# Kernel tuning notes

Measured on AMD Instinct MI355X. Metric: run time of the kernel, lower is better.

Reference implementation:

```python
import jax, jax.numpy as jnp
import numpy as np

NEG_INF = -1e9


def setup_inputs() -> dict:
    key = jax.random.key(0)
    ks = jax.random.split(key, 6)
    B, S, E, D = 32, 2048, 1024, 1024
    dec_hidden = jax.random.normal(ks[0], (B, D), dtype=jnp.float32)
    enc_outputs = jax.random.normal(ks[1], (B, S, E), dtype=jnp.float32)
    mask = jax.random.randint(ks[2], (B, S), 0, 2, dtype=jnp.int32)
    # scale weights ~ Glorot-ish so tanh isn't saturated
    W_enc = jax.random.normal(ks[3], (D, E), dtype=jnp.float32) / np.sqrt(E)
    W_dec = jax.random.normal(ks[4], (D, D), dtype=jnp.float32) / np.sqrt(D)
    v = jax.random.normal(ks[5], (D,), dtype=jnp.float32) / np.sqrt(D)
    return {"dec_hidden": dec_hidden, "enc_outputs": enc_outputs, "mask": mask,
            "W_enc": W_enc, "W_dec": W_dec, "v": v}


def reference(dec_hidden, enc_outputs, mask, W_enc, W_dec, v):
    # dh: [B, D]  (torch Linear: x @ W.T)
    dh = dec_hidden @ W_dec.T
    # eh: [B, S, D]
    eh = jnp.einsum('bse,de->bsd', enc_outputs, W_enc)
    # additive energy + projection by v -> scores [B, S]
    energy = jnp.tanh(dh[:, None, :] + eh)
    scores = jnp.einsum('bsd,d->bs', energy, v)
    scores = jnp.where(mask == 0, NEG_INF, scores)
    weights = jax.nn.softmax(scores, axis=1)          # [B, S]
    context = jnp.einsum('bs,bse->be', weights, enc_outputs)  # [B, E]
    return context, weights
```

## Files before the change

### kernel.cpp

```cpp
#include <hip/hip_runtime.h>
#include <stdint.h>

typedef float f32x4 __attribute__((ext_vector_type(4)));
typedef float f32x16 __attribute__((ext_vector_type(16)));
typedef short bf16x8 __attribute__((ext_vector_type(8)));
typedef unsigned short ushort8 __attribute__((ext_vector_type(8)));

__device__ __forceinline__ unsigned short f2bf(float x) {
  union { float f; uint32_t u; } c; c.f = x;
  return (unsigned short)((c.u + 0x8000u) >> 16);
}
__device__ __forceinline__ float bf2f(unsigned short u) {
  union { uint32_t u; float f; } c; c.u = ((uint32_t)u) << 16;
  return c.f;
}


__global__ void prep_fused_k(const float* __restrict__ W, unsigned short* __restrict__ Wt,
                             const float* __restrict__ dec, const float* __restrict__ Wd,
                             float* __restrict__ dh) {
  if (blockIdx.x < 512) {
    int t = blockIdx.x * 256 + threadIdx.x;
    int d  = t >> 7;
    int c0 = (t & 127) << 3;
    const float* src = W + ((size_t)d << 10) + c0;
    f32x4 f0 = *(const f32x4*)src;
    f32x4 f1 = *(const f32x4*)(src + 4);
    ushort8 u;
    u[0]=f2bf(f0[0]); u[1]=f2bf(f0[1]); u[2]=f2bf(f0[2]); u[3]=f2bf(f0[3]);
    u[4]=f2bf(f1[0]); u[5]=f2bf(f1[1]); u[6]=f2bf(f1[2]); u[7]=f2bf(f1[3]);
    int nt = d >> 7, r = d & 127;
    int kt = c0 >> 6, kb = (c0 & 63) >> 3;
    *(ushort8*)(Wt + ((size_t)nt << 17) + (kt << 13) + ((kb * 128 + r) << 3)) = u;
  } else {
    __shared__ float sdec[1024];
    int bb = blockIdx.x - 512;
    int b = bb >> 2;
    for (int i = threadIdx.x; i < 1024; i += 256) sdec[i] = dec[(b << 10) + i];
    __syncthreads();
    int d = ((bb & 3) << 8) + threadIdx.x;
    const float* wr = Wd + ((size_t)d << 10);
    float a = 0.f;
    for (int k = 0; k < 1024; k += 4) {
      f32x4 wv = *(const f32x4*)(wr + k);
      f32x4 xv = *(const f32x4*)(&sdec[k]);
      a += wv[0]*xv[0] + wv[1]*xv[1] + wv[2]*xv[2] + wv[3]*xv[3];
    }
    dh[(b << 10) + d] = a;
  }
}

__global__ void compact_k(const int* __restrict__ mask, int* __restrict__ rows,
                          int* __restrict__ cnt, float* __restrict__ wout) {
  int b = blockIdx.x, tid = threadIdx.x;
  int lane = tid & 63, wv = tid >> 6;
  int mloc[8]; int c = 0;
  #pragma unroll
  for (int ii = 0; ii < 8; ++ii) {
    int s = tid * 8 + ii;
    int m = mask[(b << 11) + s];
    mloc[ii] = m; c += m;
    wout[(b << 11) + s] = 0.f;
  }
  int inc = c;
  #pragma unroll
  for (int off = 1; off < 64; off <<= 1) {
    int nn = __shfl_up(inc, off);
    if (lane >= off) inc += nn;
  }
  __shared__ int wsum[4];
  if (lane == 63) wsum[wv] = inc;
  __syncthreads();
  int base = 0;
  for (int w = 0; w < wv; ++w) base += wsum[w];
  int idx = base + inc - c;
  #pragma unroll
  for (int ii = 0; ii < 8; ++ii) {
    if (mloc[ii]) { rows[(b << 11) + idx] = tid * 8 + ii; ++idx; }
  }
  if (tid == 0) cnt[b] = wsum[0] + wsum[1] + wsum[2] + wsum[3];
}

__global__ void pack8_k(const float* __restrict__ enc, const int* __restrict__ rows,
                        const int* __restrict__ cnt, unsigned short* __restrict__ encP) {
  int b = blockIdx.x >> 4, mt = blockIdx.x & 15;
  int n = cnt[b];
  if (mt * 128 >= n) return;
  __shared__ int sr[128];
  __shared__ unsigned short T[128 * 64];
  int tid = threadIdx.x;
  if (tid < 128) {
    int i = mt * 128 + tid; if (i >= n) i = n - 1;
    sr[tid] = rows[(b << 11) + i];
  }
  __syncthreads();
  unsigned short* dst = encP + (((size_t)(b * 16 + mt)) << 17);
  for (int kt = 0; kt < 16; ++kt) {
    #pragma unroll
    for (int p = 0; p < 4; ++p) {
      int id = p * 256 + tid;
      int r = id >> 3, cseg = id & 7;
      const float* src = enc + (((size_t)(b << 11) + sr[r]) << 10) + (kt << 6) + (cseg << 3);
      f32x4 f0 = *(const f32x4*)src;
      f32x4 f1 = *(const f32x4*)(src + 4);
      ushort8 u;
      u[0]=f2bf(f0[0]); u[1]=f2bf(f0[1]); u[2]=f2bf(f0[2]); u[3]=f2bf(f0[3]);
      u[4]=f2bf(f1[0]); u[5]=f2bf(f1[1]); u[6]=f2bf(f1[2]); u[7]=f2bf(f1[3]);
      *(ushort8*)&T[(r << 6) + ((cseg ^ (r & 7)) << 3)] = u;
    }
    __syncthreads();
    unsigned short* g = dst + (kt << 13);
    #pragma unroll
    for (int p = 0; p < 4; ++p) {
      int blk = p * 256 + tid;
      int kb = blk >> 7, r = blk & 127;
      ushort8 u = *(const ushort8*)&T[(r << 6) + ((kb ^ (r & 7)) << 3)];
      *(ushort8*)(g + (blk << 3)) = u;
    }
    __syncthreads();
  }
}

__global__ __launch_bounds__(256, 3) void score10_k(
    const unsigned short* __restrict__ encP, const unsigned short* __restrict__ Wt,
    const float* __restrict__ dh, const float* __restrict__ v,
    const int* __restrict__ cnt, float* __restrict__ pscores)
{
  int L  = (blockIdx.x & 7) * 512 + (blockIdx.x >> 3);
  int b  = L >> 7, mt = (L >> 3) & 15, nt = L & 7;
  int n  = cnt[b];
  if (mt * 128 >= n) return;

  __shared__ __align__(16) unsigned short AS[3][4096];
  __shared__ __align__(16) unsigned short BS[3][4096];

  int tid  = threadIdx.x;
  int lane = tid & 63;
  int wv   = tid >> 6;
  int wm = wv >> 1, wn = wv & 1;
  int l31 = lane & 31, l5 = lane >> 5;

  const unsigned short* aT = encP + (((size_t)(b * 16 + mt)) << 17);
  const unsigned short* bT = Wt + ((size_t)nt << 17);

  int offA[2][2], offB[2][2];
  #pragma unroll
  for (int mf = 0; mf < 2; ++mf) {
    int r = wm * 64 + mf * 32 + l31;
    #pragma unroll
    for (int ki = 0; ki < 2; ++ki)
      offA[mf][ki] = (((ki * 2 + l5) << 7) + r) << 3;
  }
  #pragma unroll
  for (int nf = 0; nf < 2; ++nf) {
    int r = wn * 64 + nf * 32 + l31;
    #pragma unroll
    for (int ki = 0; ki < 2; ++ki)
      offB[nf][ki] = (((ki * 2 + l5) << 7) + r) << 3;
  }

  f32x16 acc[2][2];
  #pragma unroll
  for (int i = 0; i < 2; ++i)
    #pragma unroll
    for (int j = 0; j < 2; ++j)
      #pragma unroll
      for (int e = 0; e < 16; ++e)
        acc[i][j][e] = 0.f;

  auto stage = [&](int slot, int kt) {
    #pragma unroll
    for (int j = 0; j < 2; ++j) {
      int off = j * 2048 + tid * 8;
      __builtin_amdgcn_global_load_lds(
        (const __attribute__((address_space(1))) void*)(const void*)(aT + ((size_t)kt << 12) + off),
        (__attribute__((address_space(3))) void*)(void*)(&AS[slot][off]), 16, 0, 0);
      __builtin_amdgcn_global_load_lds(
        (const __attribute__((address_space(1))) void*)(const void*)(bT + ((size_t)kt << 12) + off),
        (__attribute__((address_space(3))) void*)(void*)(&BS[slot][off]), 16, 0, 0);
    }
  };

#define VMFENCE(N) { asm volatile("s_waitcnt vmcnt(" #N ")" ::: "memory"); \
                     __builtin_amdgcn_sched_barrier(0); }
#define LKFENCE    { asm volatile("s_waitcnt lgkmcnt(0)" ::: "memory"); \
                     __builtin_amdgcn_sched_barrier(0); }
#define BARRIER    { __builtin_amdgcn_s_barrier(); __builtin_amdgcn_sched_barrier(0); }

#define KBODY(SLOT, T, SSLOT)                                              \
  {                                                                        \
    bf16x8 af[2][2], bf[2][2];                                             \
    _Pragma("unroll")                                                      \
    for (int mf = 0; mf < 2; ++mf)                                         \
      _Pragma("unroll")                                                    \
      for (int ki = 0; ki < 2; ++ki)                                       \
        af[mf][ki] = *(const bf16x8*)&AS[SLOT][offA[mf][ki]];              \
    _Pragma("unroll")                                                      \
    for (int nf = 0; nf < 2; ++nf)                                         \
      _Pragma("unroll")                                                    \
      for (int ki = 0; ki < 2; ++ki)                                       \
        bf[nf][ki] = *(const bf16x8*)&BS[SLOT][offB[nf][ki]];              \
    LKFENCE                                                                \
    stage((SSLOT), (T) + 2);                                               \
    VMFENCE(4)                                                             \
    BARRIER                                                                \
    _Pragma("unroll")                                                      \
    for (int ki = 0; ki < 2; ++ki)                                         \
      _Pragma("unroll")                                                    \
      for (int mf = 0; mf < 2; ++mf)                                       \
        _Pragma("unroll")                                                  \
        for (int nf = 0; nf < 2; ++nf)                                     \
          acc[mf][nf] = __builtin_amdgcn_mfma_f32_32x32x16_bf16(           \
              af[mf][ki], bf[nf][ki], acc[mf][nf], 0, 0, 0);               \
  }

  stage(0, 0);
  stage(1, 1);
  VMFENCE(4)
  BARRIER

  #pragma unroll 1
  for (int t = 0; t < 30; t += 3) {
    KBODY(0, t,     2)
    KBODY(1, t + 1, 0)
    KBODY(2, t + 2, 1)
  }
  {
    bf16x8 af[2][2], bf[2][2];
    #pragma unroll
    for (int mf = 0; mf < 2; ++mf)
      #pragma unroll
      for (int ki = 0; ki < 2; ++ki)
        af[mf][ki] = *(const bf16x8*)&AS[0][offA[mf][ki]];
    #pragma unroll
    for (int nf = 0; nf < 2; ++nf)
      #pragma unroll
      for (int ki = 0; ki < 2; ++ki)
        bf[nf][ki] = *(const bf16x8*)&BS[0][offB[nf][ki]];
    LKFENCE
    VMFENCE(0)
    BARRIER
    #pragma unroll
    for (int ki = 0; ki < 2; ++ki)
      #pragma unroll
      for (int mf = 0; mf < 2; ++mf)
        #pragma unroll
        for (int nf = 0; nf < 2; ++nf)
          acc[mf][nf] = __builtin_amdgcn_mfma_f32_32x32x16_bf16(af[mf][ki], bf[nf][ki], acc[mf][nf], 0, 0, 0);
  }
  {
    bf16x8 af[2][2], bf[2][2];
    #pragma unroll
    for (int mf = 0; mf < 2; ++mf)
      #pragma unroll
      for (int ki = 0; ki < 2; ++ki)
        af[mf][ki] = *(const bf16x8*)&AS[1][offA[mf][ki]];
    #pragma unroll
    for (int nf = 0; nf < 2; ++nf)
      #pragma unroll
      for (int ki = 0; ki < 2; ++ki)
        bf[nf][ki] = *(const bf16x8*)&BS[1][offB[nf][ki]];
    #pragma unroll
    for (int ki = 0; ki < 2; ++ki)
      #pragma unroll
      for (int mf = 0; mf < 2; ++mf)
        #pragma unroll
        for (int nf = 0; nf < 2; ++nf)
          acc[mf][nf] = __builtin_amdgcn_mfma_f32_32x32x16_bf16(af[mf][ki], bf[nf][ki], acc[mf][nf], 0, 0, 0);
  }
#undef KBODY

  __syncthreads();
  float* sc = (float*)AS;
  float vv[2], dd[2];
  #pragma unroll
  for (int nf = 0; nf < 2; ++nf) {
    int dcol = nt * 128 + wn * 64 + nf * 32 + l31;
    vv[nf] = v[dcol];
    dd[nf] = dh[(b << 10) + dcol];
  }
  #pragma unroll
  for (int mf = 0; mf < 2; ++mf) {
    #pragma unroll
    for (int reg = 0; reg < 16; ++reg) {
      float p = 0.f;
      #pragma unroll
      for (int nf = 0; nf < 2; ++nf) {
        float x = acc[mf][nf][reg] + dd[nf];
        float e = __expf(2.0f * x);
        float t = 1.0f - __fdividef(2.0f, e + 1.0f);
        p += vv[nf] * t;
      }
      p += __shfl_xor(p, 1); p += __shfl_xor(p, 2); p += __shfl_xor(p, 4);
      p += __shfl_xor(p, 8); p += __shfl_xor(p, 16);
      if (l31 == 0) {
        int row = wm * 64 + mf * 32 + (reg & 3) + 8 * (reg >> 2) + 4 * l5;
        sc[row * 2 + wn] = p;
      }
    }
  }
  __syncthreads();
  if (tid < 128) {
    int i = mt * 128 + tid;
    if (i < n)
      pscores[(((size_t)nt) << 16) + (b << 11) + i] = sc[tid * 2 + 0] + sc[tid * 2 + 1];
  }
}

__global__ void softmax4_k(const float* __restrict__ ps, const int* __restrict__ rows,
                           const int* __restrict__ cnt, float* __restrict__ wout,
                           float* __restrict__ wc) {
  int b = blockIdx.x;
  int tid = threadIdx.x;
  int n = cnt[b];
  float val[8];
  float m = -INFINITY;
  #pragma unroll
  for (int ii = 0; ii < 8; ++ii) {
    int i = tid + ii * 256;
    float s = -INFINITY;
    if (i < n) {
      s = 0.f;
      #pragma unroll
      for (int nt = 0; nt < 8; ++nt) s += ps[(((size_t)nt) << 16) + (b << 11) + i];
    }
    val[ii] = s;
    m = fmaxf(m, s);
  }
  #pragma unroll
  for (int off = 1; off < 64; off <<= 1) m = fmaxf(m, __shfl_xor(m, off));
  __shared__ float r1[4], r2[4];
  if ((tid & 63) == 0) r1[tid >> 6] = m;
  __syncthreads();
  m = fmaxf(fmaxf(r1[0], r1[1]), fmaxf(r1[2], r1[3]));
  float ssum = 0.f;
  #pragma unroll
  for (int ii = 0; ii < 8; ++ii) { val[ii] = __expf(val[ii] - m); ssum += val[ii]; }
  #pragma unroll
  for (int off = 1; off < 64; off <<= 1) ssum += __shfl_xor(ssum, off);
  if ((tid & 63) == 0) r2[tid >> 6] = ssum;
  __syncthreads();
  ssum = r2[0] + r2[1] + r2[2] + r2[3];
  float inv = 1.0f / ssum;
  #pragma unroll
  for (int ii = 0; ii < 8; ++ii) {
    int i = tid + ii * 256;
    if (i < n) {
      float w = val[ii] * inv;
      wc[(b << 11) + i] = w;
      wout[((size_t)b << 11) + rows[(b << 11) + i]] = w;
    }
  }
}

__global__ void ctx8_k(const unsigned short* __restrict__ encP, const float* __restrict__ wc,
                       const int* __restrict__ cnt, float* __restrict__ cp) {
  int b = blockIdx.x >> 4, mt = blockIdx.x & 15;
  int n = cnt[b];
  float* out = cp + (((size_t)(b * 16 + mt)) << 10);
  int tid = threadIdx.x;
  if (mt * 128 >= n) {
    #pragma unroll
    for (int j = 0; j < 4; ++j) out[tid * 4 + j] = 0.f;
    return;
  }
  __shared__ float sw[128];
  __shared__ float red[128][8];
  if (tid < 128) {
    int i = mt * 128 + tid;
    sw[tid] = (i < n) ? wc[(b << 11) + i] : 0.f;
  }
  __syncthreads();
  const unsigned short* tile = encP + (((size_t)(b * 16 + mt)) << 17);
  int cb8  = tid & 127;
  int half = tid >> 7;
  const unsigned short* base = tile + ((cb8 >> 3) << 13) + ((cb8 & 7) << 10);
  float a[8];
  #pragma unroll
  for (int j = 0; j < 8; ++j) a[j] = 0.f;
  for (int rr = 0; rr < 64; ++rr) {
    int r = half * 64 + rr;
    float w = sw[r];
    ushort8 u = *(const ushort8*)(base + (r << 3));
    #pragma unroll
    for (int j = 0; j < 8; ++j) a[j] += w * bf2f(u[j]);
  }
  if (half == 1) {
    #pragma unroll
    for (int j = 0; j < 8; ++j) red[cb8][j] = a[j];
  }
  __syncthreads();
  if (half == 0) {
    #pragma unroll
    for (int j = 0; j < 8; ++j) out[cb8 * 8 + j] = a[j] + red[cb8][j];
  }
}

__global__ void ctx_red4_k(const float* __restrict__ cp, float* __restrict__ out) {
  int t = blockIdx.x * 256 + threadIdx.x;
  int b = t >> 10, e = t & 1023;
  float a = 0.f;
  #pragma unroll
  for (int mt = 0; mt < 16; ++mt) a += cp[(((size_t)(b * 16 + mt)) << 10) + e];
  out[t] = a;
}

extern "C" void kernel_launch(void* const* d_in, const int* in_sizes, int n_in,
                              void* d_out, int out_size, void* d_ws, size_t ws_size,
                              hipStream_t stream) {
  const float* dec  = (const float*)d_in[0];
  const float* enc  = (const float*)d_in[1];
  const int*   mask = (const int*)d_in[2];
  const float* Wenc = (const float*)d_in[3];
  const float* Wdec = (const float*)d_in[4];
  const float* v    = (const float*)d_in[5];
  float* out_ctx = (float*)d_out;
  float* out_w   = (float*)d_out + 32768;

  char* ws = (char*)d_ws;
  unsigned short* Wt = (unsigned short*)ws;
  float* dh    = (float*)(ws + (2u << 20));
  int*   rows  = (int*)(ws + (2u << 20) + (128u << 10));
  float* wc    = (float*)(ws + (2u << 20) + (384u << 10));
  int*   cnt   = (int*)(ws + (2u << 20) + (640u << 10));
  float* pscores = (float*)(ws + (3u << 20));
  float* cp      = (float*)(ws + (5u << 20));
  unsigned short* encP = (unsigned short*)(ws + (8ull << 20));

  hipLaunchKernelGGL(prep_fused_k, dim3(640),  dim3(256), 0, stream, Wenc, Wt, dec, Wdec, dh);
  hipLaunchKernelGGL(compact_k,    dim3(32),   dim3(256), 0, stream, mask, rows, cnt, out_w);
  hipLaunchKernelGGL(pack8_k,      dim3(512),  dim3(256), 0, stream, enc, rows, cnt, encP);
  hipLaunchKernelGGL(score10_k,    dim3(4096), dim3(256), 0, stream, encP, Wt, dh, v, cnt, pscores);
  hipLaunchKernelGGL(softmax4_k,   dim3(32),   dim3(256), 0, stream, pscores, rows, cnt, out_w, wc);
  hipLaunchKernelGGL(ctx8_k,       dim3(512),  dim3(256), 0, stream, encP, wc, cnt, cp);
  hipLaunchKernelGGL(ctx_red4_k,   dim3(128),  dim3(256), 0, stream, cp, out_ctx);
}
```

Before: 198.8 us.

## Load B operand directly to registers, merge mask compaction into prep kernel

Folds the mask compaction kernel into the prep kernel as extra blocks, removing one launch. In the score GEMM, the W tile is no longer staged through LDS. It is loaded straight from global memory into double-buffered registers one K-step ahead, which halves LDS usage and may raise occupancy. The epilogue replaces per-register butterfly shuffles with a transpose-style reduction that uses fewer shuffles. The trade-off is more VGPR pressure and uncoalesced per-lane global loads for B, which rely on L2 hits.

```diff
diff --git a/kernel.cpp b/kernel.cpp
--- a/kernel.cpp
+++ b/kernel.cpp
@@ -18,7 +18,9 @@
 
 __global__ void prep_fused_k(const float* __restrict__ W, unsigned short* __restrict__ Wt,
                              const float* __restrict__ dec, const float* __restrict__ Wd,
-                             float* __restrict__ dh) {
+                             float* __restrict__ dh, const int* __restrict__ mask,
+                             int* __restrict__ rows, int* __restrict__ cnt,
+                             float* __restrict__ wout) {
   if (blockIdx.x < 512) {
     int t = blockIdx.x * 256 + threadIdx.x;
     int d  = t >> 7;
@@ -32,7 +34,7 @@
     int nt = d >> 7, r = d & 127;
     int kt = c0 >> 6, kb = (c0 & 63) >> 3;
     *(ushort8*)(Wt + ((size_t)nt << 17) + (kt << 13) + ((kb * 128 + r) << 3)) = u;
-  } else {
+  } else if (blockIdx.x < 640) {
     __shared__ float sdec[1024];
     int bb = blockIdx.x - 512;
     int b = bb >> 2;
@@ -47,38 +49,35 @@
       a += wv[0]*xv[0] + wv[1]*xv[1] + wv[2]*xv[2] + wv[3]*xv[3];
     }
     dh[(b << 10) + d] = a;
-  }
-}
-
-__global__ void compact_k(const int* __restrict__ mask, int* __restrict__ rows,
-                          int* __restrict__ cnt, float* __restrict__ wout) {
-  int b = blockIdx.x, tid = threadIdx.x;
-  int lane = tid & 63, wv = tid >> 6;
-  int mloc[8]; int c = 0;
-  #pragma unroll
-  for (int ii = 0; ii < 8; ++ii) {
-    int s = tid * 8 + ii;
-    int m = mask[(b << 11) + s];
-    mloc[ii] = m; c += m;
-    wout[(b << 11) + s] = 0.f;
-  }
-  int inc = c;
-  #pragma unroll
-  for (int off = 1; off < 64; off <<= 1) {
-    int nn = __shfl_up(inc, off);
-    if (lane >= off) inc += nn;
-  }
-  __shared__ int wsum[4];
-  if (lane == 63) wsum[wv] = inc;
-  __syncthreads();
-  int base = 0;
-  for (int w = 0; w < wv; ++w) base += wsum[w];
-  int idx = base + inc - c;
-  #pragma unroll
-  for (int ii = 0; ii < 8; ++ii) {
-    if (mloc[ii]) { rows[(b << 11) + idx] = tid * 8 + ii; ++idx; }
-  }
-  if (tid == 0) cnt[b] = wsum[0] + wsum[1] + wsum[2] + wsum[3];
+  } else {
+    int b = blockIdx.x - 640, tid = threadIdx.x;
+    int lane = tid & 63, wvx = tid >> 6;
+    int mloc[8]; int c = 0;
+    #pragma unroll
+    for (int ii = 0; ii < 8; ++ii) {
+      int s = tid * 8 + ii;
+      int m = mask[(b << 11) + s];
+      mloc[ii] = m; c += m;
+      wout[(b << 11) + s] = 0.f;
+    }
+    int inc = c;
+    #pragma unroll
+    for (int off = 1; off < 64; off <<= 1) {
+      int nn = __shfl_up(inc, off);
+      if (lane >= off) inc += nn;
+    }
+    __shared__ int wsum[4];
+    if (lane == 63) wsum[wvx] = inc;
+    __syncthreads();
+    int base = 0;
+    for (int w = 0; w < wvx; ++w) base += wsum[w];
+    int idx = base + inc - c;
+    #pragma unroll
+    for (int ii = 0; ii < 8; ++ii) {
+      if (mloc[ii]) { rows[(b << 11) + idx] = tid * 8 + ii; ++idx; }
+    }
+    if (tid == 0) cnt[b] = wsum[0] + wsum[1] + wsum[2] + wsum[3];
+  }
 }
 
 __global__ void pack8_k(const float* __restrict__ enc, const int* __restrict__ rows,
@@ -121,7 +120,7 @@
   }
 }
 
-__global__ __launch_bounds__(256, 3) void score10_k(
+__global__ __launch_bounds__(256, 3) void score12_k(
     const unsigned short* __restrict__ encP, const unsigned short* __restrict__ Wt,
     const float* __restrict__ dh, const float* __restrict__ v,
     const int* __restrict__ cnt, float* __restrict__ pscores)
@@ -132,7 +131,6 @@
   if (mt * 128 >= n) return;
 
   __shared__ __align__(16) unsigned short AS[3][4096];
-  __shared__ __align__(16) unsigned short BS[3][4096];
 
   int tid  = threadIdx.x;
   int lane = tid & 63;
@@ -143,7 +141,7 @@
   const unsigned short* aT = encP + (((size_t)(b * 16 + mt)) << 17);
   const unsigned short* bT = Wt + ((size_t)nt << 17);
 
-  int offA[2][2], offB[2][2];
+  int offA[2][2], boff[2][2];
   #pragma unroll
   for (int mf = 0; mf < 2; ++mf) {
     int r = wm * 64 + mf * 32 + l31;
@@ -156,7 +154,7 @@
     int r = wn * 64 + nf * 32 + l31;
     #pragma unroll
     for (int ki = 0; ki < 2; ++ki)
-      offB[nf][ki] = (((ki * 2 + l5) << 7) + r) << 3;
+      boff[nf][ki] = (((ki * 2 + l5) << 7) + r) << 3;
   }
 
   f32x16 acc[2][2];
@@ -168,17 +166,23 @@
       for (int e = 0; e < 16; ++e)
         acc[i][j][e] = 0.f;
 
-  auto stage = [&](int slot, int kt) {
+  auto stageA = [&](int slot, int kt) {
     #pragma unroll
     for (int j = 0; j < 2; ++j) {
       int off = j * 2048 + tid * 8;
       __builtin_amdgcn_global_load_lds(
         (const __attribute__((address_space(1))) void*)(const void*)(aT + ((size_t)kt << 12) + off),
         (__attribute__((address_space(3))) void*)(void*)(&AS[slot][off]), 16, 0, 0);
-      __builtin_amdgcn_global_load_lds(
-        (const __attribute__((address_space(1))) void*)(const void*)(bT + ((size_t)kt << 12) + off),
-        (__attribute__((address_space(3))) void*)(void*)(&BS[slot][off]), 16, 0, 0);
-    }
+    }
+  };
+
+  bf16x8 bX[2][2], bY[2][2];
+  auto loadB = [&](bf16x8 (&dst)[2][2], int kt) {
+    #pragma unroll
+    for (int nf = 0; nf < 2; ++nf)
+      #pragma unroll
+      for (int ki = 0; ki < 2; ++ki)
+        dst[nf][ki] = *(const bf16x8*)(bT + ((size_t)kt << 12) + boff[nf][ki]);
   };
 
 #define VMFENCE(N) { asm volatile("s_waitcnt vmcnt(" #N ")" ::: "memory"); \
@@ -187,22 +191,18 @@
                      __builtin_amdgcn_sched_barrier(0); }
 #define BARRIER    { __builtin_amdgcn_s_barrier(); __builtin_amdgcn_sched_barrier(0); }
 
-#define KBODY(SLOT, T, SSLOT)                                              \
+#define KBODY(SLOT, T, SSLOT, BC, BN)                                      \
   {                                                                        \
-    bf16x8 af[2][2], bf[2][2];                                             \
+    bf16x8 af[2][2];                                                       \
     _Pragma("unroll")                                                      \
     for (int mf = 0; mf < 2; ++mf)                                         \
       _Pragma("unroll")                                                    \
       for (int ki = 0; ki < 2; ++ki)                                       \
         af[mf][ki] = *(const bf16x8*)&AS[SLOT][offA[mf][ki]];              \
-    _Pragma("unroll")                                                      \
-    for (int nf = 0; nf < 2; ++nf)                                         \
-      _Pragma("unroll")                                                    \
-      for (int ki = 0; ki < 2; ++ki)                                       \
-        bf[nf][ki] = *(const bf16x8*)&BS[SLOT][offB[nf][ki]];              \
+    loadB(BN, (T) + 1);                                                    \
     LKFENCE                                                                \
-    stage((SSLOT), (T) + 2);                                               \
-    VMFENCE(4)                                                             \
+    stageA((SSLOT), (T) + 2);                                              \
+    VMFENCE(6)                                                             \
     BARRIER                                                                \
     _Pragma("unroll")                                                      \
     for (int ki = 0; ki < 2; ++ki)                                         \
@@ -211,34 +211,35 @@
         _Pragma("unroll")                                                  \
         for (int nf = 0; nf < 2; ++nf)                                     \
           acc[mf][nf] = __builtin_amdgcn_mfma_f32_32x32x16_bf16(           \
-              af[mf][ki], bf[nf][ki], acc[mf][nf], 0, 0, 0);               \
-  }
-
-  stage(0, 0);
-  stage(1, 1);
-  VMFENCE(4)
+              af[mf][ki], BC[nf][ki], acc[mf][nf], 0, 0, 0);               \
+  }
+
+  stageA(0, 0);
+  stageA(1, 1);
+  loadB(bX, 0);
+  VMFENCE(6)
   BARRIER
 
   #pragma unroll 1
-  for (int t = 0; t < 30; t += 3) {
-    KBODY(0, t,     2)
-    KBODY(1, t + 1, 0)
-    KBODY(2, t + 2, 1)
-  }
+  for (int t = 0; t < 30; t += 6) {
+    KBODY(0, t,     2, bX, bY)
+    KBODY(1, t + 1, 0, bY, bX)
+    KBODY(2, t + 2, 1, bX, bY)
+    KBODY(0, t + 3, 2, bY, bX)
+    KBODY(1, t + 4, 0, bX, bY)
+    KBODY(2, t + 5, 1, bY, bX)
+  }
+#undef KBODY
   {
-    bf16x8 af[2][2], bf[2][2];
+    bf16x8 af[2][2];
     #pragma unroll
     for (int mf = 0; mf < 2; ++mf)
       #pragma unroll
       for (int ki = 0; ki < 2; ++ki)
         af[mf][ki] = *(const bf16x8*)&AS[0][offA[mf][ki]];
-    #pragma unroll
-    for (int nf = 0; nf < 2; ++nf)
-      #pragma unroll
-      for (int ki = 0; ki < 2; ++ki)
-        bf[nf][ki] = *(const bf16x8*)&BS[0][offB[nf][ki]];
+    loadB(bY, 31);
     LKFENCE
-    VMFENCE(0)
+    VMFENCE(4)
     BARRIER
     #pragma unroll
     for (int ki = 0; ki < 2; ++ki)
@@ -246,29 +247,23 @@
       for (int mf = 0; mf < 2; ++mf)
         #pragma unroll
         for (int nf = 0; nf < 2; ++nf)
-          acc[mf][nf] = __builtin_amdgcn_mfma_f32_32x32x16_bf16(af[mf][ki], bf[nf][ki], acc[mf][nf], 0, 0, 0);
+          acc[mf][nf] = __builtin_amdgcn_mfma_f32_32x32x16_bf16(af[mf][ki], bX[nf][ki], acc[mf][nf], 0, 0, 0);
   }
   {
-    bf16x8 af[2][2], bf[2][2];
+    bf16x8 af[2][2];
     #pragma unroll
     for (int mf = 0; mf < 2; ++mf)
       #pragma unroll
       for (int ki = 0; ki < 2; ++ki)
         af[mf][ki] = *(const bf16x8*)&AS[1][offA[mf][ki]];
-    #pragma unroll
-    for (int nf = 0; nf < 2; ++nf)
-      #pragma unroll
-      for (int ki = 0; ki < 2; ++ki)
-        bf[nf][ki] = *(const bf16x8*)&BS[1][offB[nf][ki]];
     #pragma unroll
     for (int ki = 0; ki < 2; ++ki)
       #pragma unroll
       for (int mf = 0; mf < 2; ++mf)
         #pragma unroll
         for (int nf = 0; nf < 2; ++nf)
-          acc[mf][nf] = __builtin_amdgcn_mfma_f32_32x32x16_bf16(af[mf][ki], bf[nf][ki], acc[mf][nf], 0, 0, 0);
-  }
-#undef KBODY
+          acc[mf][nf] = __builtin_amdgcn_mfma_f32_32x32x16_bf16(af[mf][ki], bY[nf][ki], acc[mf][nf], 0, 0, 0);
+  }
 
   __syncthreads();
   float* sc = (float*)AS;
@@ -279,6 +274,7 @@
     vv[nf] = v[dcol];
     dd[nf] = dh[(b << 10) + dcol];
   }
+  float val[32];
   #pragma unroll
   for (int mf = 0; mf < 2; ++mf) {
     #pragma unroll
@@ -291,13 +287,21 @@
         float t = 1.0f - __fdividef(2.0f, e + 1.0f);
         p += vv[nf] * t;
       }
-      p += __shfl_xor(p, 1); p += __shfl_xor(p, 2); p += __shfl_xor(p, 4);
-      p += __shfl_xor(p, 8); p += __shfl_xor(p, 16);
-      if (l31 == 0) {
-        int row = wm * 64 + mf * 32 + (reg & 3) + 8 * (reg >> 2) + 4 * l5;
-        sc[row * 2 + wn] = p;
-      }
-    }
+      val[mf * 16 + reg] = p;
+    }
+  }
+#define RSTAGE(M, HALF)                                          \
+  _Pragma("unroll")                                              \
+  for (int j = 0; j < (HALF); ++j) {                             \
+    float keep = (l31 & (M)) ? val[(HALF) + j] : val[j];         \
+    float send = (l31 & (M)) ? val[j] : val[(HALF) + j];         \
+    val[j] = keep + __shfl_xor(send, (M));                       \
+  }
+  RSTAGE(16, 16) RSTAGE(8, 8) RSTAGE(4, 4) RSTAGE(2, 2) RSTAGE(1, 1)
+#undef RSTAGE
+  {
+    int row = wm * 64 + ((l31 >> 4) << 5) + (l31 & 3) + (((l31 >> 2) & 3) << 3) + (l5 << 2);
+    sc[row * 2 + wn] = val[0];
   }
   __syncthreads();
   if (tid < 128) {
@@ -427,10 +431,10 @@
   float* cp      = (float*)(ws + (5u << 20));
   unsigned short* encP = (unsigned short*)(ws + (8ull << 20));
 
-  hipLaunchKernelGGL(prep_fused_k, dim3(640),  dim3(256), 0, stream, Wenc, Wt, dec, Wdec, dh);
-  hipLaunchKernelGGL(compact_k,    dim3(32),   dim3(256), 0, stream, mask, rows, cnt, out_w);
+  hipLaunchKernelGGL(prep_fused_k, dim3(672),  dim3(256), 0, stream, Wenc, Wt, dec, Wdec, dh,
+                     mask, rows, cnt, out_w);
   hipLaunchKernelGGL(pack8_k,      dim3(512),  dim3(256), 0, stream, enc, rows, cnt, encP);
-  hipLaunchKernelGGL(score10_k,    dim3(4096), dim3(256), 0, stream, encP, Wt, dh, v, cnt, pscores);
+  hipLaunchKernelGGL(score12_k,    dim3(4096), dim3(256), 0, stream, encP, Wt, dh, v, cnt, pscores);
   hipLaunchKernelGGL(softmax4_k,   dim3(32),   dim3(256), 0, stream, pscores, rows, cnt, out_w, wc);
   hipLaunchKernelGGL(ctx8_k,       dim3(512),  dim3(256), 0, stream, encP, wc, cnt, cp);
   hipLaunchKernelGGL(ctx_red4_k,   dim3(128),  dim3(256), 0, stream, cp, out_ctx);
```

Measured after the change: 192.2 us. 1.03x faster.
